# Performance work log

Hardware: AMD Instinct MI355X
Metric: run time of the kernel (lower is better)

Reference implementation:

```python
import jax, jax.numpy as jnp
import numpy as np

N, E, IN_CH, C, H, L, NCLS = 4096, 131072, 512, 256, 4, 3, 2
DH = C // H  # MHA head dim


def _ln(x, g, b, eps=1e-5):
    mu = x.mean(-1, keepdims=True)
    var = ((x - mu) ** 2).mean(-1, keepdims=True)
    return (x - mu) * jax.lax.rsqrt(var + eps) * g + b


def _gelu(x):
    return jax.nn.gelu(x, approximate=False)  # torch nn.GELU default (erf)


def _gatv2(x, src, dst, wl, wr, att, b):
    # x: [N,C]; wl/wr: [H*C, C]; att: [H,C]; b: [C]
    xl = (x @ wl.T).reshape(N, H, C)  # source transform
    e = jax.nn.leaky_relu(xl[src] + (x @ wr.T).reshape(N, H, C)[dst], 0.2)  # [Et,H,C]
    score = jnp.einsum('ehc,hc->eh', e, att)  # [Et,H]
    m = jax.ops.segment_max(score, dst, num_segments=N)
    ex = jnp.exp(score - m[dst])
    denom = jax.ops.segment_sum(ex, dst, num_segments=N)
    alpha = ex / denom[dst]  # segment softmax over incoming edges
    out = jax.ops.segment_sum(alpha[:, :, None] * xl[src], dst, num_segments=N)
    return out.mean(axis=1) + b  # concat=False -> head mean


def _mha(x, in_w, in_b, out_w, out_b):
    qkv = x @ in_w.T + in_b  # [N,3C]
    q, k, v = [t.reshape(N, H, DH) for t in jnp.split(qkv, 3, axis=-1)]
    scores = jnp.einsum('nhd,mhd->hnm', q, k) / np.sqrt(DH)
    probs = jax.nn.softmax(scores, axis=-1)
    o = jnp.einsum('hnm,mhd->nhd', probs, v).reshape(N, C)
    return o @ out_w.T + out_b


def setup_inputs() -> dict:
    key = jax.random.key(0)
    ks = iter(jax.random.split(key, 64))
    s = lambda shape, sc=0.05: jax.random.normal(next(ks), shape, jnp.float32) * sc
    d = {
        'x': jax.random.normal(next(ks), (N, IN_CH), jnp.float32),
        'edge_index': jax.random.randint(next(ks), (2, E), 0, N, jnp.int32),
        'in_w': s((C, IN_CH)), 'in_b': jnp.zeros((C,), jnp.float32),
        'gat_wl': s((L, H * C, C)), 'gat_wr': s((L, H * C, C)),
        'gat_att': s((L, H, C)), 'gat_b': jnp.zeros((L, C), jnp.float32),
        'mha_in_w': s((L, 3 * C, C)), 'mha_in_b': jnp.zeros((L, 3 * C), jnp.float32),
        'mha_out_w': s((L, C, C)), 'mha_out_b': jnp.zeros((L, C), jnp.float32),
        'ln1_g': jnp.ones((L, C), jnp.float32), 'ln1_b': jnp.zeros((L, C), jnp.float32),
        'ln2_g': jnp.ones((L, C), jnp.float32), 'ln2_b': jnp.zeros((L, C), jnp.float32),
        'ln3_g': jnp.ones((L, C), jnp.float32), 'ln3_b': jnp.zeros((L, C), jnp.float32),
        'ffn_w1': s((L, 2 * C, C)), 'ffn_b1': jnp.zeros((L, 2 * C), jnp.float32),
        'ffn_w2': s((L, C, 2 * C)), 'ffn_b2': jnp.zeros((L, C), jnp.float32),
        'out_w1': s((C, C)), 'out_b1': jnp.zeros((C,), jnp.float32),
        'out_w2': s((NCLS, C)), 'out_b2': jnp.zeros((NCLS,), jnp.float32),
    }
    return d


def reference(x, edge_index, in_w, in_b, gat_wl, gat_wr, gat_att, gat_b,
              mha_in_w, mha_in_b, mha_out_w, mha_out_b,
              ln1_g, ln1_b, ln2_g, ln2_b, ln3_g, ln3_b,
              ffn_w1, ffn_b1, ffn_w2, ffn_b2,
              out_w1, out_b1, out_w2, out_b2):
    # add self loops (PyG GATv2Conv default)
    loop = jnp.arange(N, dtype=edge_index.dtype)
    src = jnp.concatenate([edge_index[0], loop])
    dst = jnp.concatenate([edge_index[1], loop])

    h = x @ in_w.T + in_b  # input_proj
    for l in range(L):
        local = _gatv2(h, src, dst, gat_wl[l], gat_wr[l], gat_att[l], gat_b[l])
        h = _ln(h + local, ln1_g[l], ln1_b[l])
        attn = _mha(h, mha_in_w[l], mha_in_b[l], mha_out_w[l], mha_out_b[l])
        h = _ln(h + attn, ln2_g[l], ln2_b[l])
        ffn = _gelu(h @ ffn_w1[l].T + ffn_b1[l]) @ ffn_w2[l].T + ffn_b2[l]
        h = _ln(h + ffn, ln3_g[l], ln3_b[l])
    h = _gelu(h @ out_w1.T + out_b1)
    return h @ out_w2.T + out_b2
```

## Files before the change

### kernel.cpp

```cpp
#include <hip/hip_runtime.h>
#include <cstdint>
#include <cstddef>

typedef unsigned short u16;
typedef __bf16 bf16x8 __attribute__((ext_vector_type(8)));
typedef float f32x4 __attribute__((ext_vector_type(4)));

constexpr int kN  = 4096;
constexpr int kE  = 131072;
constexpr int kET = kE + kN;
constexpr int kIn = 512;
constexpr int kC  = 256;
constexpr int kL  = 3;

constexpr int NSPLIT = 4;
constexpr int KSPAN  = kN / NSPLIT;
constexpr int NSTEP  = KSPAN / 64;

__device__ __forceinline__ u16 f2bf(float f) {
    unsigned u = __builtin_bit_cast(unsigned, f);
    u += 0x7fffu + ((u >> 16) & 1u);
    return (u16)(u >> 16);
}
__device__ __forceinline__ float bf2f(u16 s) {
    unsigned u = ((unsigned)s) << 16;
    return __builtin_bit_cast(float, u);
}
__device__ __forceinline__ float gelu_erf(float x) {
    return 0.5f * x * (1.f + erff(x * 0.70710678118654752f));
}
__device__ __forceinline__ void gload_lds16(const u16* gsrc, u16* ldst) {
    __builtin_amdgcn_global_load_lds(
        (const __attribute__((address_space(1))) unsigned int*)gsrc,
        (__attribute__((address_space(3))) unsigned int*)ldst, 16, 0, 0);
}
__device__ __forceinline__ float dpp_ror_add16(float x) {
    int t;
    t = __builtin_amdgcn_update_dpp(0, __builtin_bit_cast(int, x), 0x121, 0xf, 0xf, true);
    x += __builtin_bit_cast(float, t);
    t = __builtin_amdgcn_update_dpp(0, __builtin_bit_cast(int, x), 0x122, 0xf, 0xf, true);
    x += __builtin_bit_cast(float, t);
    t = __builtin_amdgcn_update_dpp(0, __builtin_bit_cast(int, x), 0x124, 0xf, 0xf, true);
    x += __builtin_bit_cast(float, t);
    t = __builtin_amdgcn_update_dpp(0, __builtin_bit_cast(int, x), 0x128, 0xf, 0xf, true);
    x += __builtin_bit_cast(float, t);
    return x;
}
__device__ __forceinline__ void unpack8(uint4 u, float* x) {
    x[0] = __builtin_bit_cast(float, u.x << 16);
    x[1] = __builtin_bit_cast(float, u.x & 0xffff0000u);
    x[2] = __builtin_bit_cast(float, u.y << 16);
    x[3] = __builtin_bit_cast(float, u.y & 0xffff0000u);
    x[4] = __builtin_bit_cast(float, u.z << 16);
    x[5] = __builtin_bit_cast(float, u.z & 0xffff0000u);
    x[6] = __builtin_bit_cast(float, u.w << 16);
    x[7] = __builtin_bit_cast(float, u.w & 0xffff0000u);
}

__global__ void cast_all(
    const float* __restrict__ x, const float* __restrict__ in_w,
    const float* __restrict__ gwl, const float* __restrict__ gwr,
    const float* __restrict__ minw, const float* __restrict__ moutw,
    const float* __restrict__ f1, const float* __restrict__ f2,
    const float* __restrict__ o1,
    u16* __restrict__ xbf, u16* __restrict__ wbf) {
    int i = blockIdx.x * 256 + threadIdx.x;
    if (i >= 1359872) return;
    const float* s;
    u16* dbase;
    int sj, dj;
    if (i < 524288) {
        s = x; dbase = xbf; sj = i; dj = i;
    } else if (i < 557056) {
        s = in_w; dbase = wbf; sj = i - 524288; dj = sj;
    } else if (i < 753664) {
        int j = i - 557056; int l = j >> 16, wi = j & 65535;
        s = gwl; dbase = wbf; sj = j; dj = 32768 + l * 131072 + wi;
    } else if (i < 950272) {
        int j = i - 753664; int l = j >> 16, wi = j & 65535;
        s = gwr; dbase = wbf; sj = j; dj = 32768 + l * 131072 + 65536 + wi;
    } else if (i < 1097728) {
        s = minw; dbase = wbf; sj = i - 950272; dj = 425984 + sj;
    } else if (i < 1146880) {
        s = moutw; dbase = wbf; sj = i - 1097728; dj = 573440 + sj;
    } else if (i < 1245184) {
        s = f1; dbase = wbf; sj = i - 1146880; dj = 622592 + sj;
    } else if (i < 1343488) {
        s = f2; dbase = wbf; sj = i - 1245184; dj = 720896 + sj;
    } else {
        s = o1; dbase = wbf; sj = i - 1343488; dj = 819200 + sj;
    }
    float4 v = ((const float4*)s)[sj];
    ushort4 o;
    o.x = f2bf(v.x); o.y = f2bf(v.y); o.z = f2bf(v.z); o.w = f2bf(v.w);
    ((ushort4*)dbase)[dj] = o;
}

__global__ void csr_count(const int* __restrict__ ei, int* __restrict__ cnt) {
    int e = blockIdx.x * 256 + threadIdx.x;
    if (e >= kET) return;
    int d = (e < kE) ? ei[kE + e] : (e - kE);
    atomicAdd(cnt + d, 1);
}

__global__ __launch_bounds__(1024) void csr_scan(int* __restrict__ cnt_cur, int* __restrict__ off) {
    __shared__ int lds[1024];
    int t = threadIdx.x;
    int c[4], s = 0;
#pragma unroll
    for (int j = 0; j < 4; ++j) { c[j] = cnt_cur[t * 4 + j]; s += c[j]; }
    lds[t] = s;
    __syncthreads();
    for (int d = 1; d < 1024; d <<= 1) {
        int v = (t >= d) ? lds[t - d] : 0;
        __syncthreads();
        lds[t] += v;
        __syncthreads();
    }
    int excl = lds[t] - s;
#pragma unroll
    for (int j = 0; j < 4; ++j) { off[t * 4 + j] = excl; cnt_cur[t * 4 + j] = excl; excl += c[j]; }
    if (t == 1023) off[4096] = excl;
}

__global__ void csr_scatter(const int* __restrict__ ei, int* __restrict__ cur, int* __restrict__ csrc) {
    int e = blockIdx.x * 256 + threadIdx.x;
    if (e >= kET) return;
    int s, d;
    if (e < kE) { s = ei[e]; d = ei[kE + e]; } else { s = d = e - kE; }
    int pos = atomicAdd(cur + d, 1);
    csrc[pos] = s;
}

template <int BM, int K, int ACT, int WF32, int WBF16>
__global__ __launch_bounds__(256) void gemm_st(
    const u16* __restrict__ A, const u16* __restrict__ W,
    const float* __restrict__ bias, float* __restrict__ Cf,
    u16* __restrict__ Cb, int N) {
    constexpr int BK = 32;
    constexpr int NK = K / BK;
    constexpr int MF = BM / 32;
    int tid = threadIdx.x;
    int w = tid >> 6, lane = tid & 63;
    int wr = w >> 1, wc = w & 1;
    int g = lane >> 4, r = lane & 15;
    int bm = blockIdx.y * BM;
    int bn = blockIdx.x * 64;
    __shared__ __align__(16) u16 Ab[2][BM * BK];
    __shared__ __align__(16) u16 Bb[2][64 * BK];
    int srow = w * 16 + (lane >> 2);
    int scol = (lane & 3) * 8;
    auto stage = [&](int buf, int k0) {
#pragma unroll
        for (int i = 0; i < BM / 64; ++i)
            gload_lds16(A + (size_t)(bm + i * 64 + srow) * K + k0 + scol,
                        &Ab[buf][(i * 64 + w * 16) * BK]);
        gload_lds16(W + (size_t)(bn + srow) * K + k0 + scol, &Bb[buf][w * 16 * BK]);
    };
    f32x4 acc[MF][2] = {};
    stage(0, 0);
    __syncthreads();
    for (int st = 0; st < NK; ++st) {
        int cur = st & 1;
        if (st + 1 < NK) stage(cur ^ 1, (st + 1) * BK);
        const u16* Al = &Ab[cur][0];
        const u16* Bl = &Bb[cur][0];
        bf16x8 bf[2];
#pragma unroll
        for (int u = 0; u < 2; ++u)
            bf[u] = *(const bf16x8*)(Bl + (wc * 32 + u * 16 + r) * BK + g * 8);
#pragma unroll
        for (int t = 0; t < MF; ++t) {
            bf16x8 af = *(const bf16x8*)(Al + (wr * (BM / 2) + t * 16 + r) * BK + g * 8);
#pragma unroll
            for (int u = 0; u < 2; ++u)
                acc[t][u] = __builtin_amdgcn_mfma_f32_16x16x32_bf16(af, bf[u], acc[t][u], 0, 0, 0);
        }
        __syncthreads();
    }
    int r0 = bm + wr * (BM / 2) + g * 4;
    int c0 = bn + wc * 32 + r;
#pragma unroll
    for (int t = 0; t < MF; ++t)
#pragma unroll
        for (int u = 0; u < 2; ++u)
#pragma unroll
            for (int e = 0; e < 4; ++e) {
                int row = r0 + t * 16 + e, col = c0 + u * 16;
                float v = acc[t][u][e];
                if (bias) v += bias[col];
                if (ACT == 1) v = gelu_erf(v);
                if (WF32) Cf[(size_t)row * N + col] = v;
                if (WBF16) Cb[(size_t)row * N + col] = f2bf(v);
            }
}

__global__ __launch_bounds__(256) void gemm_qkv(
    const u16* __restrict__ A, const u16* __restrict__ W,
    const float* __restrict__ bias,
    u16* __restrict__ Qb, u16* __restrict__ Kb, u16* __restrict__ VTb) {
    constexpr int BK = 32, K = 256, NK = 8, BM = 128, MF = 4;
    int tid = threadIdx.x;
    int w = tid >> 6, lane = tid & 63;
    int wr = w >> 1, wc = w & 1;
    int g = lane >> 4, r = lane & 15;
    int bm = blockIdx.y * BM;
    int bn = blockIdx.x * 64;
    __shared__ __align__(16) u16 Ab[2][BM * BK];
    __shared__ __align__(16) u16 Bb[2][64 * BK];
    int srow = w * 16 + (lane >> 2);
    int scol = (lane & 3) * 8;
    auto stage = [&](int buf, int k0) {
#pragma unroll
        for (int i = 0; i < 2; ++i)
            gload_lds16(A + (size_t)(bm + i * 64 + srow) * K + k0 + scol,
                        &Ab[buf][(i * 64 + w * 16) * BK]);
        gload_lds16(W + (size_t)(bn + srow) * K + k0 + scol, &Bb[buf][w * 16 * BK]);
    };
    f32x4 acc[MF][2] = {};
    stage(0, 0);
    __syncthreads();
    for (int st = 0; st < NK; ++st) {
        int cur = st & 1;
        if (st + 1 < NK) stage(cur ^ 1, (st + 1) * BK);
        const u16* Al = &Ab[cur][0];
        const u16* Bl = &Bb[cur][0];
        bf16x8 bf[2];
#pragma unroll
        for (int u = 0; u < 2; ++u)
            bf[u] = *(const bf16x8*)(Bl + (wc * 32 + u * 16 + r) * BK + g * 8);
#pragma unroll
        for (int t = 0; t < MF; ++t) {
            bf16x8 af = *(const bf16x8*)(Al + (wr * 64 + t * 16 + r) * BK + g * 8);
#pragma unroll
            for (int u = 0; u < 2; ++u)
                acc[t][u] = __builtin_amdgcn_mfma_f32_16x16x32_bf16(af, bf[u], acc[t][u], 0, 0, 0);
        }
        __syncthreads();
    }
    constexpr float QS = 0.125f * 1.4426950408889634f;
    int region = blockIdx.x >> 2;
    int head = blockIdx.x & 3;
    int r0 = bm + wr * 64 + g * 4;
    if (region == 2) {
#pragma unroll
        for (int t = 0; t < MF; ++t)
#pragma unroll
            for (int u = 0; u < 2; ++u) {
                int d = wc * 32 + u * 16 + r;
                int col = bn + d;
                ushort4 vo;
                vo.x = f2bf(acc[t][u][0] + bias[col]);
                vo.y = f2bf(acc[t][u][1] + bias[col]);
                vo.z = f2bf(acc[t][u][2] + bias[col]);
                vo.w = f2bf(acc[t][u][3] + bias[col]);
                *(ushort4*)(VTb + ((size_t)head * 64 + d) * kN + r0 + t * 16) = vo;
            }
    } else {
        u16* dst = (region == 0) ? Qb : Kb;
        float sc = (region == 0) ? QS : 1.f;
#pragma unroll
        for (int t = 0; t < MF; ++t)
#pragma unroll
            for (int u = 0; u < 2; ++u)
#pragma unroll
                for (int e = 0; e < 4; ++e) {
                    int d = wc * 32 + u * 16 + r;
                    int row = r0 + t * 16 + e;
                    dst[((size_t)head * kN + row) * 64 + d] =
                        f2bf((acc[t][u][e] + bias[bn + d]) * sc);
                }
    }
}

template <int K>
__global__ __launch_bounds__(256) void gemm_128(
    const u16* __restrict__ A, const u16* __restrict__ W,
    u16* __restrict__ Cb, int N) {
    constexpr int BK = 32;
    constexpr int NK = K / BK;
    int tid = threadIdx.x;
    int w = tid >> 6, lane = tid & 63;
    int wr = w >> 1, wc = w & 1;
    int g = lane >> 4, r = lane & 15;
    int bm = blockIdx.y * 128;
    int bn = blockIdx.x * 128;
    __shared__ __align__(16) u16 Ab[2][128 * BK];
    __shared__ __align__(16) u16 Bb[2][128 * BK];
    int srd = lane >> 2;
    int schunk = ((lane & 3) ^ ((lane >> 3) & 3)) * 8;
    auto stage = [&](int buf, int k0) {
#pragma unroll
        for (int i = 0; i < 2; ++i) {
            int rowA = bm + i * 64 + w * 16 + srd;
            int rowB = bn + i * 64 + w * 16 + srd;
            gload_lds16(A + (size_t)rowA * K + k0 + schunk, &Ab[buf][(i * 64 + w * 16) * BK]);
            gload_lds16(W + (size_t)rowB * K + k0 + schunk, &Bb[buf][(i * 64 + w * 16) * BK]);
        }
    };
    f32x4 acc[4][4] = {};
    stage(0, 0);
    __syncthreads();
    int rs = (r >> 1) & 3;
    for (int st = 0; st < NK; ++st) {
        int cur = st & 1;
        if (st + 1 < NK) stage(cur ^ 1, (st + 1) * BK);
        const u16* Al = &Ab[cur][0];
        const u16* Bl = &Bb[cur][0];
        bf16x8 bf[4];
#pragma unroll
        for (int u = 0; u < 4; ++u)
            bf[u] = *(const bf16x8*)(Bl + (wc * 64 + u * 16 + r) * BK + ((g ^ rs) * 8));
#pragma unroll
        for (int t = 0; t < 4; ++t) {
            bf16x8 af = *(const bf16x8*)(Al + (wr * 64 + t * 16 + r) * BK + ((g ^ rs) * 8));
#pragma unroll
            for (int u = 0; u < 4; ++u)
                acc[t][u] = __builtin_amdgcn_mfma_f32_16x16x32_bf16(af, bf[u], acc[t][u], 0, 0, 0);
        }
        __syncthreads();
    }
#pragma unroll
    for (int t = 0; t < 4; ++t)
#pragma unroll
        for (int u = 0; u < 4; ++u)
#pragma unroll
            for (int e = 0; e < 4; ++e) {
                int row = bm + wr * 64 + t * 16 + g * 4 + e;
                int col = bn + wc * 64 + u * 16 + r;
                Cb[(size_t)row * N + col] = f2bf(acc[t][u][e]);
            }
}

template <int BM, int K>
__global__ __launch_bounds__(256) void gemm_ln(
    const u16* __restrict__ A, const u16* __restrict__ W,
    const float* __restrict__ bias,
    const float* __restrict__ lng, const float* __restrict__ lnb,
    float* __restrict__ h, u16* __restrict__ hbf) {
    constexpr int BK = 32;
    constexpr int NK = K / BK;
    constexpr int MT = BM / 16;
    int tid = threadIdx.x;
    int w = tid >> 6, lane = tid & 63;
    int g = lane >> 4, r = lane & 15;
    int bm = blockIdx.x * BM;
    __shared__ __align__(16) u16 Ab[2][BM * BK];
    __shared__ __align__(16) u16 Bb[2][256 * BK];
    __shared__ float sums[BM][4][2];
    int srd = lane >> 2;
    int schunk = ((lane & 3) ^ ((lane >> 3) & 3)) * 8;
    auto stage = [&](int buf, int k0) {
        if (w < MT)
            gload_lds16(A + (size_t)(bm + w * 16 + srd) * K + k0 + schunk,
                        &Ab[buf][(w * 16) * BK]);
#pragma unroll
        for (int i = 0; i < 4; ++i)
            gload_lds16(W + (size_t)(w * 64 + i * 16 + srd) * K + k0 + schunk,
                        &Bb[buf][(w * 64 + i * 16) * BK]);
    };
    f32x4 acc[MT][4] = {};
    stage(0, 0);
    __syncthreads();
    int rs = (r >> 1) & 3;
    for (int st = 0; st < NK; ++st) {
        int cur = st & 1;
        if (st + 1 < NK) stage(cur ^ 1, (st + 1) * BK);
        const u16* Al = &Ab[cur][0];
        const u16* Bl = &Bb[cur][0];
        bf16x8 bf[4];
#pragma unroll
        for (int u = 0; u < 4; ++u)
            bf[u] = *(const bf16x8*)(Bl + (w * 64 + u * 16 + r) * BK + ((g ^ rs) * 8));
#pragma unroll
        for (int t = 0; t < MT; ++t) {
            bf16x8 af = *(const bf16x8*)(Al + (t * 16 + r) * BK + ((g ^ rs) * 8));
#pragma unroll
            for (int u = 0; u < 4; ++u)
                acc[t][u] = __builtin_amdgcn_mfma_f32_16x16x32_bf16(af, bf[u], acc[t][u], 0, 0, 0);
        }
        __syncthreads();
    }
    float val[MT][4][4];
#pragma unroll
    for (int t = 0; t < MT; ++t)
#pragma unroll
        for (int e = 0; e < 4; ++e) {
            int row = bm + t * 16 + g * 4 + e;
            float s1 = 0.f, s2 = 0.f;
#pragma unroll
            for (int u = 0; u < 4; ++u) {
                int col = w * 64 + u * 16 + r;
                float v = acc[t][u][e] + bias[col] + h[(size_t)row * kC + col];
                val[t][u][e] = v;
                s1 += v;
                s2 += v * v;
            }
            s1 = dpp_ror_add16(s1);
            s2 = dpp_ror_add16(s2);
            if (r == 0) {
                sums[t * 16 + g * 4 + e][w][0] = s1;
                sums[t * 16 + g * 4 + e][w][1] = s2;
            }
        }
    __syncthreads();
#pragma unroll
    for (int t = 0; t < MT; ++t)
#pragma unroll
        for (int e = 0; e < 4; ++e) {
            int lr = t * 16 + g * 4 + e;
            int row = bm + lr;
            float S1 = sums[lr][0][0] + sums[lr][1][0] + sums[lr][2][0] + sums[lr][3][0];
            float S2 = sums[lr][0][1] + sums[lr][1][1] + sums[lr][2][1] + sums[lr][3][1];
            float mu = S1 * (1.f / kC);
            float rstd = rsqrtf(S2 * (1.f / kC) - mu * mu + 1e-5f);
#pragma unroll
            for (int u = 0; u < 4; ++u) {
                int col = w * 64 + u * 16 + r;
                float y = (val[t][u][e] - mu) * rstd * lng[col] + lnb[col];
                h[(size_t)row * kC + col] = y;
                hbf[(size_t)row * kC + col] = f2bf(y);
            }
        }
}

__global__ __launch_bounds__(256) void gat_agg(
    const u16* __restrict__ xg,
    const float* __restrict__ att, const float* __restrict__ gb,
    const int* __restrict__ off, const int* __restrict__ srcs,
    const float* __restrict__ lng, const float* __restrict__ lnb,
    float* __restrict__ h, u16* __restrict__ hbf) {
    int n = blockIdx.x;
    int w = threadIdx.x >> 6, lane = threadIdx.x & 63;
    int q = lane >> 4, t = lane & 15;
    int cb = w * 256 + t * 16;

    uint4 xru0 = *(const uint4*)(xg + (size_t)n * 2048 + 1024 + cb);
    uint4 xru1 = *(const uint4*)(xg + (size_t)n * 2048 + 1024 + cb + 8);
    float xrv[16];
    unpack8(xru0, xrv); unpack8(xru1, xrv + 8);
    float att6[16], att4[16];
#pragma unroll
    for (int j = 0; j < 16; j += 4) {
        float4 a4 = *(const float4*)(att + cb + j);
        att6[j] = 0.6f * a4.x; att6[j + 1] = 0.6f * a4.y;
        att6[j + 2] = 0.6f * a4.z; att6[j + 3] = 0.6f * a4.w;
        att4[j] = (2.f / 3.f) * att6[j]; att4[j + 1] = (2.f / 3.f) * att6[j + 1];
        att4[j + 2] = (2.f / 3.f) * att6[j + 2]; att4[j + 3] = (2.f / 3.f) * att6[j + 3];
    }

    int i0 = off[n], i1 = off[n + 1];
    float m = -1e30f, ls = 0.f;
    float acc[16] = {};
    int i = i0 + q;
    uint4 p0a, p1a, p0b, p1b;
    if (i < i1) {
        int s = srcs[i];
        p0a = *(const uint4*)(xg + (size_t)s * 2048 + cb);
        p1a = *(const uint4*)(xg + (size_t)s * 2048 + cb + 8);
    }
    if (i + 4 < i1) {
        int s = srcs[i + 4];
        p0b = *(const uint4*)(xg + (size_t)s * 2048 + cb);
        p1b = *(const uint4*)(xg + (size_t)s * 2048 + cb + 8);
    }
    while (i < i1) {
        uint4 c0 = p0a, c1 = p1a;
        p0a = p0b; p1a = p1b;
        if (i + 8 < i1) {
            int s2 = srcs[i + 8];
            p0b = *(const uint4*)(xg + (size_t)s2 * 2048 + cb);
            p1b = *(const uint4*)(xg + (size_t)s2 * 2048 + cb + 8);
        }
        float x[16];
        unpack8(c0, x); unpack8(c1, x + 8);
        float pp[4] = {0.f, 0.f, 0.f, 0.f};
#pragma unroll
        for (int j = 0; j < 16; ++j) {
            float e = x[j] + xrv[j];
            pp[j & 3] = fmaf(att6[j], e, pp[j & 3]);
            pp[j & 3] = fmaf(att4[j], __builtin_fabsf(e), pp[j & 3]);
        }
        float p = dpp_ror_add16((pp[0] + pp[1]) + (pp[2] + pp[3]));
        if (p > m) {
            float c = __expf(m - p);
            ls = ls * c + 1.f;
#pragma unroll
            for (int j = 0; j < 16; ++j) acc[j] = acc[j] * c + x[j];
            m = p;
        } else {
            float pw = __expf(p - m);
            ls += pw;
#pragma unroll
            for (int j = 0; j < 16; ++j) acc[j] = fmaf(pw, x[j], acc[j]);
        }
        i += 4;
    }
    float mm = fmaxf(m, __shfl_xor(m, 16));
    mm = fmaxf(mm, __shfl_xor(mm, 32));
    float c = __expf(m - mm);
    ls *= c;
    ls += __shfl_xor(ls, 16);
    ls += __shfl_xor(ls, 32);
#pragma unroll
    for (int j = 0; j < 16; ++j) {
        float a = acc[j] * c;
        a += __shfl_xor(a, 16);
        a += __shfl_xor(a, 32);
        acc[j] = a;
    }
    float inv = 1.f / ls;
    __shared__ float red[4][256];
    __shared__ float rs[8];
    if (q == 0) {
#pragma unroll
        for (int j = 0; j < 16; ++j) red[w][t * 16 + j] = acc[j] * inv;
    }
    __syncthreads();
    int cc = threadIdx.x;
    float vsum = 0.25f * (red[0][cc] + red[1][cc] + red[2][cc] + red[3][cc]) + gb[cc];
    float v = h[(size_t)n * kC + cc] + vsum;
    float s1 = v, s2 = v * v;
    for (int d = 1; d < 64; d <<= 1) { s1 += __shfl_xor(s1, d); s2 += __shfl_xor(s2, d); }
    if (lane == 0) { rs[w] = s1; rs[4 + w] = s2; }
    __syncthreads();
    s1 = rs[0] + rs[1] + rs[2] + rs[3];
    s2 = rs[4] + rs[5] + rs[6] + rs[7];
    float mu = s1 * (1.f / kC);
    float rstd = rsqrtf(s2 * (1.f / kC) - mu * mu + 1e-5f);
    float y = (v - mu) * rstd * lng[cc] + lnb[cc];
    h[(size_t)n * kC + cc] = y;
    hbf[(size_t)n * kC + cc] = f2bf(y);
}

__global__ __launch_bounds__(256, 4) void mha_mfma2(
    const u16* __restrict__ Qb, const u16* __restrict__ Kb,
    const u16* __restrict__ VTb, float* __restrict__ opart, float* __restrict__ mlpart) {
    int qt = blockIdx.x, head = blockIdx.y, sp = blockIdx.z;
    int tid = threadIdx.x;
    int w = tid >> 6, lane = tid & 63;
    int g = lane >> 4, r = lane & 15;
    int q0 = qt * 64;
    const u16* Qh = Qb + ((size_t)head * kN + q0 + w * 16) * 64;
    const u16* Kh = Kb + (size_t)head * kN * 64;
    const u16* VTh = VTb + (size_t)head * 64 * kN;
    __shared__ u16 Kt[2][64 * 64];
    __shared__ u16 Vt[2][64 * 64];
    __shared__ u16 plds[4][16 * 64];
    int srow = w * 8 + (lane >> 3);
    int schunk = ((lane & 7) ^ ((lane >> 3) & 7)) * 8;
    int kbase = sp * KSPAN;

    bf16x8 qf0 = *(const bf16x8*)(Qh + r * 64 + g * 8);
    bf16x8 qf1 = *(const bf16x8*)(Qh + r * 64 + 32 + g * 8);

    auto stage = [&](int buf, int k0) {
#pragma unroll
        for (int i = 0; i < 2; ++i) {
            int row = i * 32 + srow;
            gload_lds16(Kh + (size_t)(k0 + row) * 64 + schunk, &Kt[buf][(i * 32 + w * 8) * 64]);
            gload_lds16(VTh + (size_t)row * kN + k0 + schunk, &Vt[buf][(i * 32 + w * 8) * 64]);
        }
    };

    f32x4 o[4] = {};
    float m = -3.0e38f, l = 0.f;

    stage(0, kbase);
    __syncthreads();

    int rx = r & 7;
    for (int st = 0; st < NSTEP; ++st) {
        int cur = st & 1;
        if (st + 1 < NSTEP) stage(cur ^ 1, kbase + (st + 1) * 64);
        const u16* Kl = &Kt[cur][0];
        const u16* Vl = &Vt[cur][0];
        f32x4 stt[4] = {};
#pragma unroll
        for (int t = 0; t < 4; ++t) {
            bf16x8 kf0 = *(const bf16x8*)(Kl + (16 * t + r) * 64 + ((0 + g) ^ rx) * 8);
            bf16x8 kf1 = *(const bf16x8*)(Kl + (16 * t + r) * 64 + ((4 + g) ^ rx) * 8);
            stt[t] = __builtin_amdgcn_mfma_f32_16x16x32_bf16(kf0, qf0, stt[t], 0, 0, 0);
            stt[t] = __builtin_amdgcn_mfma_f32_16x16x32_bf16(kf1, qf1, stt[t], 0, 0, 0);
        }
        float pm = stt[0][0];
#pragma unroll
        for (int t = 0; t < 4; ++t)
#pragma unroll
            for (int e = 0; e < 4; ++e) pm = fmaxf(pm, stt[t][e]);
        pm = fmaxf(pm, __shfl_xor(pm, 16));
        pm = fmaxf(pm, __shfl_xor(pm, 32));
        if (__any(pm > m)) {
            float mn = fmaxf(m, pm);
            float corr = __builtin_amdgcn_exp2f(m - mn);
            l *= corr;
            float corrq[4];
#pragma unroll
            for (int e = 0; e < 4; ++e) corrq[e] = __shfl(corr, g * 4 + e);
#pragma unroll
            for (int dt = 0; dt < 4; ++dt)
#pragma unroll
                for (int e = 0; e < 4; ++e) o[dt][e] *= corrq[e];
            m = mn;
        }
        float ls = 0.f;
        float p[4][4];
#pragma unroll
        for (int t = 0; t < 4; ++t)
#pragma unroll
            for (int e = 0; e < 4; ++e) { p[t][e] = __builtin_amdgcn_exp2f(stt[t][e] - m); ls += p[t][e]; }
        ls += __shfl_xor(ls, 16);
        ls += __shfl_xor(ls, 32);
        l += ls;
#pragma unroll
        for (int t = 0; t < 4; ++t) {
            ushort4 pk;
            pk.x = f2bf(p[t][0]); pk.y = f2bf(p[t][1]);
            pk.z = f2bf(p[t][2]); pk.w = f2bf(p[t][3]);
            int lc = (2 * t + (g >> 1)) ^ rx;
            *(ushort4*)(&plds[w][r * 64 + lc * 8 + (g & 1) * 4]) = pk;
        }
        bf16x8 pa0 = *(const bf16x8*)(&plds[w][r * 64 + (g ^ rx) * 8]);
        bf16x8 pa1 = *(const bf16x8*)(&plds[w][r * 64 + ((4 + g) ^ rx) * 8]);
#pragma unroll
        for (int dt = 0; dt < 4; ++dt) {
            bf16x8 vf0 = *(const bf16x8*)(Vl + (dt * 16 + r) * 64 + ((0 + g) ^ rx) * 8);
            bf16x8 vf1 = *(const bf16x8*)(Vl + (dt * 16 + r) * 64 + ((4 + g) ^ rx) * 8);
            o[dt] = __builtin_amdgcn_mfma_f32_16x16x32_bf16(pa0, vf0, o[dt], 0, 0, 0);
            o[dt] = __builtin_amdgcn_mfma_f32_16x16x32_bf16(pa1, vf1, o[dt], 0, 0, 0);
        }
        __syncthreads();
    }

    size_t slot = (size_t)(head * 64 + qt) * NSPLIT + sp;
    float* ob = opart + slot * 4096;
#pragma unroll
    for (int dt = 0; dt < 4; ++dt)
#pragma unroll
        for (int e = 0; e < 4; ++e)
            ob[(w * 16 + g * 4 + e) * 64 + dt * 16 + r] = o[dt][e];
    float* mlb = mlpart + slot * 128;
    if (g == 0) { mlb[w * 16 + r] = m; mlb[64 + w * 16 + r] = l; }
}

__global__ __launch_bounds__(256) void mha_merge(
    const float* __restrict__ opart, const float* __restrict__ mlpart,
    u16* __restrict__ attnb) {
    int head = blockIdx.y;
    int q = blockIdx.x * 4 + (threadIdx.x >> 6);
    int d = threadIdx.x & 63;
    int qt = q >> 6, ql = q & 63;
    size_t sb = (size_t)(head * 64 + qt) * NSPLIT;
    float ms[NSPLIT], lsv[NSPLIT];
    float mstar = -3.0e38f;
#pragma unroll
    for (int s = 0; s < NSPLIT; ++s) {
        ms[s] = mlpart[(sb + s) * 128 + ql];
        lsv[s] = mlpart[(sb + s) * 128 + 64 + ql];
        mstar = fmaxf(mstar, ms[s]);
    }
    float acc = 0.f, lsum = 0.f;
#pragma unroll
    for (int s = 0; s < NSPLIT; ++s) {
        float wgt = __builtin_amdgcn_exp2f(ms[s] - mstar);
        lsum += lsv[s] * wgt;
        acc += opart[(sb + s) * 4096 + ql * 64 + d] * wgt;
    }
    attnb[(size_t)q * kC + head * 64 + d] = f2bf(acc / lsum);
}

__global__ __launch_bounds__(256) void final_out(
    const u16* __restrict__ tbf, const float* __restrict__ w2,
    const float* __restrict__ b2, float* __restrict__ out) {
    int row = blockIdx.x * 4 + (threadIdx.x >> 6);
    int lane = threadIdx.x & 63;
    const ushort4 tv = *(const ushort4*)(tbf + (size_t)row * 256 + lane * 4);
    float t0 = bf2f(tv.x), t1 = bf2f(tv.y), t2 = bf2f(tv.z), t3 = bf2f(tv.w);
    const float4 w0 = *(const float4*)(w2 + lane * 4);
    const float4 w1 = *(const float4*)(w2 + 256 + lane * 4);
    float d0 = t0 * w0.x + t1 * w0.y + t2 * w0.z + t3 * w0.w;
    float d1 = t0 * w1.x + t1 * w1.y + t2 * w1.z + t3 * w1.w;
    for (int d = 1; d < 64; d <<= 1) { d0 += __shfl_xor(d0, d); d1 += __shfl_xor(d1, d); }
    if (lane == 0) {
        out[(size_t)row * 2 + 0] = d0 + b2[0];
        out[(size_t)row * 2 + 1] = d1 + b2[1];
    }
}

extern "C" void kernel_launch(void* const* d_in, const int* in_sizes, int n_in,
                              void* d_out, int out_size, void* d_ws, size_t ws_size,
                              hipStream_t stream) {
    (void)in_sizes; (void)n_in; (void)out_size;
    const float* x        = (const float*)d_in[0];
    const int*   ei       = (const int*)d_in[1];
    const float* in_w     = (const float*)d_in[2];
    const float* in_b     = (const float*)d_in[3];
    const float* gat_wl   = (const float*)d_in[4];
    const float* gat_wr   = (const float*)d_in[5];
    const float* gat_att  = (const float*)d_in[6];
    const float* gat_b    = (const float*)d_in[7];
    const float* mha_in_w = (const float*)d_in[8];
    const float* mha_in_b = (const float*)d_in[9];
    const float* mha_out_w= (const float*)d_in[10];
    const float* mha_out_b= (const float*)d_in[11];
    const float* ln1_g = (const float*)d_in[12];
    const float* ln1_b = (const float*)d_in[13];
    const float* ln2_g = (const float*)d_in[14];
    const float* ln2_b = (const float*)d_in[15];
    const float* ln3_g = (const float*)d_in[16];
    const float* ln3_b = (const float*)d_in[17];
    const float* ffn_w1 = (const float*)d_in[18];
    const float* ffn_b1 = (const float*)d_in[19];
    const float* ffn_w2 = (const float*)d_in[20];
    const float* ffn_b2 = (const float*)d_in[21];
    const float* out_w1 = (const float*)d_in[22];
    const float* out_b1 = (const float*)d_in[23];
    const float* out_w2 = (const float*)d_in[24];
    const float* out_b2 = (const float*)d_in[25];
    float* out = (float*)d_out;

    char* ws = (char*)d_ws;
    size_t off = 0;
    auto alloc = [&](size_t bytes) -> void* {
        void* p = (void*)(ws + off);
        off += (bytes + 255) & ~(size_t)255;
        return p;
    };
    float* h     = (float*)alloc((size_t)kN * kC * 4);
    u16*   hbf   = (u16*)  alloc((size_t)kN * kC * 2);
    float* xlb   = (float*)alloc((size_t)kN * 1024 * 4);
    float* xrb   = (float*)alloc((size_t)kN * 1024 * 4);
    float* locb  = (float*)alloc((size_t)kN * kC * 4);
    u16*   attnb = (u16*)  alloc((size_t)kN * kC * 2);
    u16*   midb  = (u16*)  alloc((size_t)kN * 512 * 2);
    u16*   tbf   = (u16*)  alloc((size_t)kN * kC * 2);
    u16*   xbf   = (u16*)  alloc((size_t)kN * kIn * 2);
    u16*   wbf   = (u16*)  alloc((size_t)3342336 * 2);
    int*   coff  = (int*)  alloc((size_t)4097 * 4);
    int*   ccur  = (int*)  alloc((size_t)4096 * 4);
    int*   csrc  = (int*)  alloc((size_t)kET * 4);
    if (ws_size < off) return;

    u16* xgbf = (u16*)xlb;
    u16* Qb  = (u16*)xlb;
    u16* Kb  = Qb + (size_t)4 * kN * 64;
    u16* VTb = Kb + (size_t)4 * kN * 64;
    float* opart  = xrb;
    float* mlpart = locb;

    const size_t OFF_INW  = 0;
    const size_t OFF_GAT  = 131072;
    const size_t OFF_MIN  = 1703936;
    const size_t OFF_MOUT = 2293760;
    const size_t OFF_F1   = 2490368;
    const size_t OFF_F2   = 2883584;
    const size_t OFF_O1   = 3276800;

    cast_all<<<dim3((1359872 + 255) / 256), dim3(256), 0, stream>>>(
        x, in_w, gat_wl, gat_wr, mha_in_w, mha_out_w, ffn_w1, ffn_w2, out_w1,
        xbf, wbf);

    hipMemsetAsync(ccur, 0, 4096 * 4, stream);
    csr_count<<<dim3((kET + 255) / 256), dim3(256), 0, stream>>>(ei, ccur);
    csr_scan<<<dim3(1), dim3(1024), 0, stream>>>(ccur, coff);
    csr_scatter<<<dim3((kET + 255) / 256), dim3(256), 0, stream>>>(ei, ccur, csrc);

    gemm_st<64, 512, 0, 1, 1><<<dim3(kC / 64, kN / 64), dim3(256), 0, stream>>>(
        xbf, wbf + OFF_INW, in_b, h, hbf, kC);

    for (int l = 0; l < kL; ++l) {
        gemm_128<256><<<dim3(2048 / 128, kN / 128), dim3(256), 0, stream>>>(
            hbf, wbf + OFF_GAT + (size_t)l * 524288, xgbf, 2048);
        gat_agg<<<dim3(kN), dim3(256), 0, stream>>>(
            xgbf, gat_att + (size_t)l * 1024, gat_b + (size_t)l * kC, coff, csrc,
            ln1_g + (size_t)l * kC, ln1_b + (size_t)l * kC, h, hbf);

        gemm_qkv<<<dim3(768 / 64, kN / 128), dim3(256), 0, stream>>>(
            hbf, wbf + OFF_MIN + (size_t)l * 768 * kC, mha_in_b + (size_t)l * 768,
            Qb, Kb, VTb);
        mha_mfma2<<<dim3(kN / 64, 4, NSPLIT), dim3(256), 0, stream>>>(Qb, Kb, VTb, opart, mlpart);
        mha_merge<<<dim3(kN / 4, 4), dim3(256), 0, stream>>>(opart, mlpart, attnb);
        gemm_ln<16, 256><<<dim3(kN / 16), dim3(256), 0, stream>>>(
            attnb, wbf + OFF_MOUT + (size_t)l * kC * kC, mha_out_b + (size_t)l * kC,
            ln2_g + (size_t)l * kC, ln2_b + (size_t)l * kC, h, hbf);

        gemm_st<64, 256, 1, 0, 1><<<dim3(512 / 64, kN / 64), dim3(256), 0, stream>>>(
            hbf, wbf + OFF_F1 + (size_t)l * 512 * kC, ffn_b1 + (size_t)l * 512, nullptr, midb, 512);
        gemm_ln<16, 512><<<dim3(kN / 16), dim3(256), 0, stream>>>(
            midb, wbf + OFF_F2 + (size_t)l * kC * 512, ffn_b2 + (size_t)l * kC,
            ln3_g + (size_t)l * kC, ln3_b + (size_t)l * kC, h, hbf);
    }

    gemm_st<64, 256, 1, 0, 1><<<dim3(kC / 64, kN / 64), dim3(256), 0, stream>>>(
        hbf, wbf + OFF_O1, out_b1, nullptr, tbf, kC);
    final_out<<<dim3(kN / 4), dim3(256), 0, stream>>>(tbf, out_w2, out_b2, out);
}
```

Measured before the change: 479.0 us.

## Process two query tiles per MHA block to reuse staged K/V tiles

The flash-attention kernel now handles 128 queries per block, two 16-row query fragments per wave, so every K/V tile staged into LDS feeds twice the MFMA work. This halves global K/V loads and the grid size. The partial-output layout and the merge kernel are re-indexed to match. Launch bounds drop to 2 waves per SIMD to allow the extra registers, which lowers occupancy. Separately, the GAT score dot product now uses a single accumulator chain instead of four partial sums, which shortens the reduction but lengthens the dependency chain.

Result: no change. 477.2 us (-0.4%).

```diff
diff --git a/kernel.cpp b/kernel.cpp
--- a/kernel.cpp
+++ b/kernel.cpp
@@ -474,14 +474,14 @@
         }
         float x[16];
         unpack8(c0, x); unpack8(c1, x + 8);
-        float pp[4] = {0.f, 0.f, 0.f, 0.f};
+        float p = 0.f;
 #pragma unroll
         for (int j = 0; j < 16; ++j) {
             float e = x[j] + xrv[j];
-            pp[j & 3] = fmaf(att6[j], e, pp[j & 3]);
-            pp[j & 3] = fmaf(att4[j], __builtin_fabsf(e), pp[j & 3]);
-        }
-        float p = dpp_ror_add16((pp[0] + pp[1]) + (pp[2] + pp[3]));
+            p = fmaf(att6[j], e, p);
+            p = fmaf(att4[j], __builtin_fabsf(e), p);
+        }
+        p = dpp_ror_add16(p);
         if (p > m) {
             float c = __expf(m - p);
             ls = ls * c + 1.f;
@@ -533,26 +533,29 @@
     hbf[(size_t)n * kC + cc] = f2bf(y);
 }
 
-__global__ __launch_bounds__(256, 4) void mha_mfma2(
+__global__ __launch_bounds__(256, 2) void mha_mfma3(
     const u16* __restrict__ Qb, const u16* __restrict__ Kb,
     const u16* __restrict__ VTb, float* __restrict__ opart, float* __restrict__ mlpart) {
     int qt = blockIdx.x, head = blockIdx.y, sp = blockIdx.z;
     int tid = threadIdx.x;
     int w = tid >> 6, lane = tid & 63;
     int g = lane >> 4, r = lane & 15;
-    int q0 = qt * 64;
-    const u16* Qh = Qb + ((size_t)head * kN + q0 + w * 16) * 64;
+    int q0 = qt * 128;
+    const u16* QhA = Qb + ((size_t)head * kN + q0 + w * 16) * 64;
+    const u16* QhB = QhA + (size_t)64 * 64;
     const u16* Kh = Kb + (size_t)head * kN * 64;
     const u16* VTh = VTb + (size_t)head * 64 * kN;
     __shared__ u16 Kt[2][64 * 64];
     __shared__ u16 Vt[2][64 * 64];
-    __shared__ u16 plds[4][16 * 64];
+    __shared__ u16 plds[4][2][16 * 64];
     int srow = w * 8 + (lane >> 3);
     int schunk = ((lane & 7) ^ ((lane >> 3) & 7)) * 8;
     int kbase = sp * KSPAN;
 
-    bf16x8 qf0 = *(const bf16x8*)(Qh + r * 64 + g * 8);
-    bf16x8 qf1 = *(const bf16x8*)(Qh + r * 64 + 32 + g * 8);
+    bf16x8 qfA0 = *(const bf16x8*)(QhA + r * 64 + g * 8);
+    bf16x8 qfA1 = *(const bf16x8*)(QhA + r * 64 + 32 + g * 8);
+    bf16x8 qfB0 = *(const bf16x8*)(QhB + r * 64 + g * 8);
+    bf16x8 qfB1 = *(const bf16x8*)(QhB + r * 64 + 32 + g * 8);
 
     auto stage = [&](int buf, int k0) {
 #pragma unroll
@@ -563,8 +566,8 @@
         }
     };
 
-    f32x4 o[4] = {};
-    float m = -3.0e38f, l = 0.f;
+    f32x4 oA[4] = {}, oB[4] = {};
+    float mA = -3.0e38f, lA = 0.f, mB = -3.0e38f, lB = 0.f;
 
     stage(0, kbase);
     __syncthreads();
@@ -575,72 +578,130 @@
         if (st + 1 < NSTEP) stage(cur ^ 1, kbase + (st + 1) * 64);
         const u16* Kl = &Kt[cur][0];
         const u16* Vl = &Vt[cur][0];
-        f32x4 stt[4] = {};
-#pragma unroll
-        for (int t = 0; t < 4; ++t) {
-            bf16x8 kf0 = *(const bf16x8*)(Kl + (16 * t + r) * 64 + ((0 + g) ^ rx) * 8);
-            bf16x8 kf1 = *(const bf16x8*)(Kl + (16 * t + r) * 64 + ((4 + g) ^ rx) * 8);
-            stt[t] = __builtin_amdgcn_mfma_f32_16x16x32_bf16(kf0, qf0, stt[t], 0, 0, 0);
-            stt[t] = __builtin_amdgcn_mfma_f32_16x16x32_bf16(kf1, qf1, stt[t], 0, 0, 0);
-        }
-        float pm = stt[0][0];
-#pragma unroll
-        for (int t = 0; t < 4; ++t)
-#pragma unroll
-            for (int e = 0; e < 4; ++e) pm = fmaxf(pm, stt[t][e]);
-        pm = fmaxf(pm, __shfl_xor(pm, 16));
-        pm = fmaxf(pm, __shfl_xor(pm, 32));
-        if (__any(pm > m)) {
-            float mn = fmaxf(m, pm);
-            float corr = __builtin_amdgcn_exp2f(m - mn);
-            l *= corr;
-            float corrq[4];
-#pragma unroll
-            for (int e = 0; e < 4; ++e) corrq[e] = __shfl(corr, g * 4 + e);
-#pragma unroll
-            for (int dt = 0; dt < 4; ++dt)
-#pragma unroll
-                for (int e = 0; e < 4; ++e) o[dt][e] *= corrq[e];
-            m = mn;
-        }
-        float ls = 0.f;
-        float p[4][4];
-#pragma unroll
-        for (int t = 0; t < 4; ++t)
-#pragma unroll
-            for (int e = 0; e < 4; ++e) { p[t][e] = __builtin_amdgcn_exp2f(stt[t][e] - m); ls += p[t][e]; }
-        ls += __shfl_xor(ls, 16);
-        ls += __shfl_xor(ls, 32);
-        l += ls;
-#pragma unroll
-        for (int t = 0; t < 4; ++t) {
-            ushort4 pk;
-            pk.x = f2bf(p[t][0]); pk.y = f2bf(p[t][1]);
-            pk.z = f2bf(p[t][2]); pk.w = f2bf(p[t][3]);
-            int lc = (2 * t + (g >> 1)) ^ rx;
-            *(ushort4*)(&plds[w][r * 64 + lc * 8 + (g & 1) * 4]) = pk;
-        }
-        bf16x8 pa0 = *(const bf16x8*)(&plds[w][r * 64 + (g ^ rx) * 8]);
-        bf16x8 pa1 = *(const bf16x8*)(&plds[w][r * 64 + ((4 + g) ^ rx) * 8]);
+        {
+            f32x4 stt[4] = {};
+#pragma unroll
+            for (int t = 0; t < 4; ++t) {
+                bf16x8 kf0 = *(const bf16x8*)(Kl + (16 * t + r) * 64 + ((0 + g) ^ rx) * 8);
+                bf16x8 kf1 = *(const bf16x8*)(Kl + (16 * t + r) * 64 + ((4 + g) ^ rx) * 8);
+                stt[t] = __builtin_amdgcn_mfma_f32_16x16x32_bf16(kf0, qfA0, stt[t], 0, 0, 0);
+                stt[t] = __builtin_amdgcn_mfma_f32_16x16x32_bf16(kf1, qfA1, stt[t], 0, 0, 0);
+            }
+            float pm = stt[0][0];
+#pragma unroll
+            for (int t = 0; t < 4; ++t)
+#pragma unroll
+                for (int e = 0; e < 4; ++e) pm = fmaxf(pm, stt[t][e]);
+            pm = fmaxf(pm, __shfl_xor(pm, 16));
+            pm = fmaxf(pm, __shfl_xor(pm, 32));
+            if (__any(pm > mA)) {
+                float mn = fmaxf(mA, pm);
+                float corr = __builtin_amdgcn_exp2f(mA - mn);
+                lA *= corr;
+                float corrq[4];
+#pragma unroll
+                for (int e = 0; e < 4; ++e) corrq[e] = __shfl(corr, g * 4 + e);
+#pragma unroll
+                for (int dt = 0; dt < 4; ++dt)
+#pragma unroll
+                    for (int e = 0; e < 4; ++e) oA[dt][e] *= corrq[e];
+                mA = mn;
+            }
+            float lsx = 0.f;
+#pragma unroll
+            for (int t = 0; t < 4; ++t) {
+                ushort4 pk;
+                float p0 = __builtin_amdgcn_exp2f(stt[t][0] - mA);
+                float p1 = __builtin_amdgcn_exp2f(stt[t][1] - mA);
+                float p2 = __builtin_amdgcn_exp2f(stt[t][2] - mA);
+                float p3 = __builtin_amdgcn_exp2f(stt[t][3] - mA);
+                lsx += (p0 + p1) + (p2 + p3);
+                pk.x = f2bf(p0); pk.y = f2bf(p1); pk.z = f2bf(p2); pk.w = f2bf(p3);
+                int lc = (2 * t + (g >> 1)) ^ rx;
+                *(ushort4*)(&plds[w][0][r * 64 + lc * 8 + (g & 1) * 4]) = pk;
+            }
+            lsx += __shfl_xor(lsx, 16);
+            lsx += __shfl_xor(lsx, 32);
+            lA += lsx;
+        }
+        {
+            f32x4 stt[4] = {};
+#pragma unroll
+            for (int t = 0; t < 4; ++t) {
+                bf16x8 kf0 = *(const bf16x8*)(Kl + (16 * t + r) * 64 + ((0 + g) ^ rx) * 8);
+                bf16x8 kf1 = *(const bf16x8*)(Kl + (16 * t + r) * 64 + ((4 + g) ^ rx) * 8);
+                stt[t] = __builtin_amdgcn_mfma_f32_16x16x32_bf16(kf0, qfB0, stt[t], 0, 0, 0);
+                stt[t] = __builtin_amdgcn_mfma_f32_16x16x32_bf16(kf1, qfB1, stt[t], 0, 0, 0);
+            }
+            float pm = stt[0][0];
+#pragma unroll
+            for (int t = 0; t < 4; ++t)
+#pragma unroll
+                for (int e = 0; e < 4; ++e) pm = fmaxf(pm, stt[t][e]);
+            pm = fmaxf(pm, __shfl_xor(pm, 16));
+            pm = fmaxf(pm, __shfl_xor(pm, 32));
+            if (__any(pm > mB)) {
+                float mn = fmaxf(mB, pm);
+                float corr = __builtin_amdgcn_exp2f(mB - mn);
+                lB *= corr;
+                float corrq[4];
+#pragma unroll
+                for (int e = 0; e < 4; ++e) corrq[e] = __shfl(corr, g * 4 + e);
+#pragma unroll
+                for (int dt = 0; dt < 4; ++dt)
+#pragma unroll
+                    for (int e = 0; e < 4; ++e) oB[dt][e] *= corrq[e];
+                mB = mn;
+            }
+            float lsx = 0.f;
+#pragma unroll
+            for (int t = 0; t < 4; ++t) {
+                ushort4 pk;
+                float p0 = __builtin_amdgcn_exp2f(stt[t][0] - mB);
+                float p1 = __builtin_amdgcn_exp2f(stt[t][1] - mB);
+                float p2 = __builtin_amdgcn_exp2f(stt[t][2] - mB);
+                float p3 = __builtin_amdgcn_exp2f(stt[t][3] - mB);
+                lsx += (p0 + p1) + (p2 + p3);
+                pk.x = f2bf(p0); pk.y = f2bf(p1); pk.z = f2bf(p2); pk.w = f2bf(p3);
+                int lc = (2 * t + (g >> 1)) ^ rx;
+                *(ushort4*)(&plds[w][1][r * 64 + lc * 8 + (g & 1) * 4]) = pk;
+            }
+            lsx += __shfl_xor(lsx, 16);
+            lsx += __shfl_xor(lsx, 32);
+            lB += lsx;
+        }
+        bf16x8 paA0 = *(const bf16x8*)(&plds[w][0][r * 64 + (g ^ rx) * 8]);
+        bf16x8 paA1 = *(const bf16x8*)(&plds[w][0][r * 64 + ((4 + g) ^ rx) * 8]);
+        bf16x8 paB0 = *(const bf16x8*)(&plds[w][1][r * 64 + (g ^ rx) * 8]);
+        bf16x8 paB1 = *(const bf16x8*)(&plds[w][1][r * 64 + ((4 + g) ^ rx) * 8]);
 #pragma unroll
         for (int dt = 0; dt < 4; ++dt) {
             bf16x8 vf0 = *(const bf16x8*)(Vl + (dt * 16 + r) * 64 + ((0 + g) ^ rx) * 8);
             bf16x8 vf1 = *(const bf16x8*)(Vl + (dt * 16 + r) * 64 + ((4 + g) ^ rx) * 8);
-            o[dt] = __builtin_amdgcn_mfma_f32_16x16x32_bf16(pa0, vf0, o[dt], 0, 0, 0);
-            o[dt] = __builtin_amdgcn_mfma_f32_16x16x32_bf16(pa1, vf1, o[dt], 0, 0, 0);
+            oA[dt] = __builtin_amdgcn_mfma_f32_16x16x32_bf16(paA0, vf0, oA[dt], 0, 0, 0);
+            oA[dt] = __builtin_amdgcn_mfma_f32_16x16x32_bf16(paA1, vf1, oA[dt], 0, 0, 0);
+            oB[dt] = __builtin_amdgcn_mfma_f32_16x16x32_bf16(paB0, vf0, oB[dt], 0, 0, 0);
+            oB[dt] = __builtin_amdgcn_mfma_f32_16x16x32_bf16(paB1, vf1, oB[dt], 0, 0, 0);
         }
         __syncthreads();
     }
 
-    size_t slot = (size_t)(head * 64 + qt) * NSPLIT + sp;
-    float* ob = opart + slot * 4096;
+    size_t slot = (size_t)(head * 32 + qt) * NSPLIT + sp;
+    float* ob = opart + slot * 8192;
 #pragma unroll
     for (int dt = 0; dt < 4; ++dt)
 #pragma unroll
-        for (int e = 0; e < 4; ++e)
-            ob[(w * 16 + g * 4 + e) * 64 + dt * 16 + r] = o[dt][e];
-    float* mlb = mlpart + slot * 128;
-    if (g == 0) { mlb[w * 16 + r] = m; mlb[64 + w * 16 + r] = l; }
+        for (int e = 0; e < 4; ++e) {
+            ob[(w * 16 + g * 4 + e) * 64 + dt * 16 + r] = oA[dt][e];
+            ob[(64 + w * 16 + g * 4 + e) * 64 + dt * 16 + r] = oB[dt][e];
+        }
+    float* mlb = mlpart + slot * 256;
+    if (g == 0) {
+        mlb[w * 16 + r] = mA;
+        mlb[64 + w * 16 + r] = mB;
+        mlb[128 + w * 16 + r] = lA;
+        mlb[192 + w * 16 + r] = lB;
+    }
 }
 
 __global__ __launch_bounds__(256) void mha_merge(
@@ -649,14 +710,14 @@
     int head = blockIdx.y;
     int q = blockIdx.x * 4 + (threadIdx.x >> 6);
     int d = threadIdx.x & 63;
-    int qt = q >> 6, ql = q & 63;
-    size_t sb = (size_t)(head * 64 + qt) * NSPLIT;
+    int qt = q >> 7, ql = q & 127;
+    size_t sb = (size_t)(head * 32 + qt) * NSPLIT;
     float ms[NSPLIT], lsv[NSPLIT];
     float mstar = -3.0e38f;
 #pragma unroll
     for (int s = 0; s < NSPLIT; ++s) {
-        ms[s] = mlpart[(sb + s) * 128 + ql];
-        lsv[s] = mlpart[(sb + s) * 128 + 64 + ql];
+        ms[s] = mlpart[(sb + s) * 256 + ql];
+        lsv[s] = mlpart[(sb + s) * 256 + 128 + ql];
         mstar = fmaxf(mstar, ms[s]);
     }
     float acc = 0.f, lsum = 0.f;
@@ -664,7 +725,7 @@
     for (int s = 0; s < NSPLIT; ++s) {
         float wgt = __builtin_amdgcn_exp2f(ms[s] - mstar);
         lsum += lsv[s] * wgt;
-        acc += opart[(sb + s) * 4096 + ql * 64 + d] * wgt;
+        acc += opart[(sb + s) * 8192 + ql * 64 + d] * wgt;
     }
     attnb[(size_t)q * kC + head * 64 + d] = f2bf(acc / lsum);
 }
@@ -778,7 +839,7 @@
         gemm_qkv<<<dim3(768 / 64, kN / 128), dim3(256), 0, stream>>>(
             hbf, wbf + OFF_MIN + (size_t)l * 768 * kC, mha_in_b + (size_t)l * 768,
             Qb, Kb, VTb);
-        mha_mfma2<<<dim3(kN / 64, 4, NSPLIT), dim3(256), 0, stream>>>(Qb, Kb, VTb, opart, mlpart);
+        mha_mfma3<<<dim3(kN / 128, 4, NSPLIT), dim3(256), 0, stream>>>(Qb, Kb, VTb, opart, mlpart);
         mha_merge<<<dim3(kN / 4, 4), dim3(256), 0, stream>>>(opart, mlpart, attnb);
         gemm_ln<16, 256><<<dim3(kN / 16), dim3(256), 0, stream>>>(
             attnb, wbf + OFF_MOUT + (size_t)l * kC * kC, mha_out_b + (size_t)l * kC,
```
